# Performance work log

Measured on AMD Instinct MI355X. Metric: run time of the kernel, lower is better.

## Reference

```python
import jax, jax.numpy as jnp
import numpy as np

# ---- static config (from init_kwargs) ----
B_, L_, DM = 4, 2048, 1024
EXPAND, HEADDIM, DSTATE, DCONV = 2, 64, 64, 7
DIN = EXPAND * DM            # 2048
NH = DIN // HEADDIM          # 32
CONV_DIM = DIN + 2 * DSTATE  # 2176 (x, B, C go through the depthwise conv)
DPROJ = 2 * DIN + 2 * DSTATE + 2 * NH  # 4288 (z, xBC, dt_fwd, dt_bwd)
EPS = 1e-5


def setup_inputs() -> dict:
    key = jax.random.key(0)
    ks = jax.random.split(key, 8)
    s = lambda d: 1.0 / np.sqrt(d)
    # dt_bias = inv_softplus(dt) with dt ~ logUniform(1e-3, 0.1)  (Mamba2/Hydra init)
    dt = jnp.exp(jax.random.uniform(ks[3], (NH,)) * (np.log(0.1) - np.log(0.001)) + np.log(0.001))
    return {
        "x": jax.random.normal(ks[0], (B_, L_, DM), jnp.float32),
        "ln_gamma": jnp.ones((DM,), jnp.float32),
        "ln_beta": jnp.zeros((DM,), jnp.float32),
        "W_in": jax.random.normal(ks[1], (DPROJ, DM), jnp.float32) * s(DM),
        "conv_w": jax.random.normal(ks[2], (CONV_DIM, DCONV), jnp.float32) * s(DCONV),
        "conv_b": jnp.zeros((CONV_DIM,), jnp.float32),
        "dt_bias": jnp.log(jnp.expm1(dt)),
        "A_log": jnp.log(jax.random.uniform(ks[4], (NH,), minval=1.0, maxval=16.0)),
        "fc_D_w": jax.random.normal(ks[5], (NH, DIN), jnp.float32) * s(DIN),
        "D": jnp.ones((NH,), jnp.float32),
        "norm_w": jnp.ones((DIN,), jnp.float32),
        "W_out": jax.random.normal(ks[6], (DM, DIN), jnp.float32) * s(DIN),
    }


def _hydra_layer(x, ln_gamma, ln_beta, W_in, conv_w, conv_b, dt_bias, A_log,
                 fc_D_w, D, norm_w, W_out):
    res = x
    # LayerNorm
    mu = jnp.mean(x, -1, keepdims=True)
    var = jnp.mean((x - mu) ** 2, -1, keepdims=True)
    u = (x - mu) * jax.lax.rsqrt(var + EPS) * ln_gamma + ln_beta

    # input projection -> z (gate), xBC (conv stream), dt (fwd+bwd)
    zxbcdt = jnp.einsum('bld,pd->blp', u, W_in)
    z = zxbcdt[..., :DIN]
    xBC = zxbcdt[..., DIN:DIN + CONV_DIM]
    dt = zxbcdt[..., DIN + CONV_DIM:]               # (B,L,2*NH)

    # depthwise 'same' conv along L + SiLU (bidirectional model -> symmetric pad)
    xBC_c = jax.lax.conv_general_dilated(
        xBC.transpose(0, 2, 1), conv_w[:, None, :], (1,),
        [(DCONV // 2, DCONV // 2)], feature_group_count=CONV_DIM)
    xBC = jax.nn.silu((xBC_c + conv_b[None, :, None]).transpose(0, 2, 1))

    xs = xBC[..., :DIN]                             # (B,L,DIN)
    Bm = xBC[..., DIN:DIN + DSTATE]                 # (B,L,N)
    Cm = xBC[..., DIN + DSTATE:]                    # (B,L,N)

    flip = lambda a: a[:, ::-1]
    # stack forward and (flipped) backward direction along batch
    dt2 = jax.nn.softplus(jnp.concatenate([dt[..., :NH], flip(dt[..., NH:])], 0) + dt_bias)  # (2B,L,NH)
    x2 = jnp.concatenate([xs, flip(xs)], 0).reshape(2 * B_, L_, NH, HEADDIM)
    B2 = jnp.concatenate([Bm, flip(Bm)], 0)
    C2 = jnp.concatenate([Cm, flip(Cm)], 0)

    A = -jnp.exp(A_log)                             # (NH,)
    dA = jnp.exp(dt2 * A)                           # (2B,L,NH)

    # selective SSM recurrence: h_t = dA_t * h_{t-1} + dt_t * x_t B_t^T ; y_t = h_t C_t
    def step(h, inp):
        dA_t, dt_t, B_t, C_t, x_t = inp
        dBx = (dt_t[:, :, None, None] * x_t[..., None]) * B_t[:, None, None, :]
        h = dA_t[:, :, None, None] * h + dBx        # (2B,NH,P,N)
        y = jnp.einsum('bhpn,bn->bhp', h, C_t)
        return h, y

    h0 = jnp.zeros((2 * B_, NH, HEADDIM, DSTATE), x.dtype)
    tr = lambda a: jnp.moveaxis(a, 1, 0)
    _, ys = jax.lax.scan(step, h0, (tr(dA), tr(dt2), tr(B2), tr(C2), tr(x2)))
    y = jnp.moveaxis(ys, 0, 1)                      # (2B,L,NH,P)

    # shift by one: strictly off-diagonal part of the quasiseparable mixing matrix
    y = jnp.concatenate([jnp.zeros_like(y[:, :1]), y[:, :-1]], axis=1)
    y = y[:B_] + flip(y[B_:])                       # (B,L,NH,P)

    # data-dependent diagonal: D(x) = fc_D(x) + D, applied per head
    Ddata = jnp.einsum('bld,hd->blh', xs, fc_D_w) + D
    y = y + xs.reshape(B_, L_, NH, HEADDIM) * Ddata[..., None]
    y = y.reshape(B_, L_, DIN)

    # gated RMSNorm (norm after gate)
    y = y * jax.nn.silu(z)
    y = y * jax.lax.rsqrt(jnp.mean(y * y, -1, keepdims=True) + EPS) * norm_w

    # out proj + residual (dropout is identity in eval)
    return res + jnp.einsum('bli,di->bld', y, W_out)


def reference(x, ln_gamma, ln_beta, W_in, conv_w, conv_b, dt_bias, A_log,
              fc_D_w, D, norm_w, W_out):
    return _hydra_layer(x, ln_gamma, ln_beta, W_in, conv_w, conv_b, dt_bias,
                        A_log, fc_D_w, D, norm_w, W_out)
```

## Files before the change

kernel.cpp:

```cpp
#include <hip/hip_runtime.h>
#include <stdint.h>

#define B_   4
#define L_   2048
#define DM   1024
#define DIN  2048
#define NH   32
#define HD   64
#define DSTATE 64
#define DCONV  7
#define CONV_DIM 2176
#define DPROJ 4288
#define NPAD 4352
#define BL   8192
#define EPS  1e-5f
#define QC   128
#define NCH  16

typedef unsigned short u16;
typedef unsigned int   u32;
typedef __bf16 bf16x8 __attribute__((ext_vector_type(8)));
typedef float  f32x4  __attribute__((ext_vector_type(4)));

__device__ __forceinline__ float b2f(u32 b) { return __uint_as_float(b << 16); }
__device__ __forceinline__ u16 f2b(float f) {
    u32 u = __float_as_uint(f);
    u32 r = (u + 0x7fffu + ((u >> 16) & 1u)) >> 16;
    return (u16)r;
}
__device__ __forceinline__ void unpack8(uint4 v, float* f) {
    f[0] = b2f(v.x & 0xffffu); f[1] = b2f(v.x >> 16);
    f[2] = b2f(v.y & 0xffffu); f[3] = b2f(v.y >> 16);
    f[4] = b2f(v.z & 0xffffu); f[5] = b2f(v.z >> 16);
    f[6] = b2f(v.w & 0xffffu); f[7] = b2f(v.w >> 16);
}
__device__ __forceinline__ uint4 pack8(const float* f) {
    uint4 v;
    v.x = (u32)f2b(f[0]) | ((u32)f2b(f[1]) << 16);
    v.y = (u32)f2b(f[2]) | ((u32)f2b(f[3]) << 16);
    v.z = (u32)f2b(f[4]) | ((u32)f2b(f[5]) << 16);
    v.w = (u32)f2b(f[6]) | ((u32)f2b(f[7]) << 16);
    return v;
}
__device__ __forceinline__ int xts(int p, int s) { return p * 136 + ((p >> 3) << 3) + s; }
__device__ __forceinline__ void gload_lds16(const u16* g, u16* l) {
    __builtin_amdgcn_global_load_lds((const __attribute__((address_space(1))) void*)g,
                                     (__attribute__((address_space(3))) void*)l, 16, 0, 0);
}

__global__ __launch_bounds__(256) void k_cvt_win(const float* __restrict__ W, u16* __restrict__ Wb) {
    int idx = blockIdx.x * 256 + threadIdx.x;
    int n = idx >> 10;
    float v = (n < DPROJ) ? W[(size_t)n * DM + (idx & 1023)] : 0.f;
    Wb[idx] = f2b(v);
}
__global__ __launch_bounds__(256) void k_cvt_wout(const float* __restrict__ W, u16* __restrict__ Wb) {
    int idx = blockIdx.x * 256 + threadIdx.x;
    Wb[idx] = f2b(W[idx]);
}
__global__ __launch_bounds__(256) void k_cvt_fcd(const float* __restrict__ W, u16* __restrict__ Wb) {
    int idx = blockIdx.x * 256 + threadIdx.x;
    Wb[idx] = f2b(W[idx]);
}

__global__ __launch_bounds__(256) void k_ln(const float* __restrict__ x, const float* __restrict__ g,
                                            const float* __restrict__ be, u16* __restrict__ u) {
    int row = blockIdx.x, tid = threadIdx.x;
    const float4* xr = (const float4*)(x + (size_t)row * DM);
    float4 v = xr[tid];
    float s1 = v.x + v.y + v.z + v.w;
    float s2 = v.x * v.x + v.y * v.y + v.z * v.z + v.w * v.w;
    for (int o = 32; o; o >>= 1) { s1 += __shfl_down(s1, o); s2 += __shfl_down(s2, o); }
    __shared__ float ls1[4], ls2[4];
    int w = tid >> 6;
    if ((tid & 63) == 0) { ls1[w] = s1; ls2[w] = s2; }
    __syncthreads();
    float t1 = ls1[0] + ls1[1] + ls1[2] + ls1[3];
    float t2 = ls2[0] + ls2[1] + ls2[2] + ls2[3];
    float mu = t1 * (1.f / DM);
    float var = t2 * (1.f / DM) - mu * mu;
    float rs = rsqrtf(var + EPS);
    float4 gv = ((const float4*)g)[tid];
    float4 bv = ((const float4*)be)[tid];
    float o0 = (v.x - mu) * rs * gv.x + bv.x;
    float o1 = (v.y - mu) * rs * gv.y + bv.y;
    float o2 = (v.z - mu) * rs * gv.z + bv.z;
    float o3 = (v.w - mu) * rs * gv.w + bv.w;
    uint2 p;
    p.x = (u32)f2b(o0) | ((u32)f2b(o1) << 16);
    p.y = (u32)f2b(o2) | ((u32)f2b(o3) << 16);
    ((uint2*)(u + (size_t)row * DM))[tid] = p;
}

#define G256_ITER(VMLIT, STG, tcur)                                              \
  {                                                                              \
    asm volatile("s_waitcnt vmcnt(" #VMLIT ")" ::: "memory");                    \
    __builtin_amdgcn_s_barrier();                                                \
    asm volatile("" ::: "memory");                                               \
    const int b_ = (tcur) & 3;                                                   \
    bf16x8 bf_[4], af_[4];                                                       \
    _Pragma("unroll")                                                            \
    for (int nj = 0; nj < 4; nj++) bf_[nj] = *(const bf16x8*)&Bs[b_][rdB + nj * 512]; \
    _Pragma("unroll")                                                            \
    for (int mi = 0; mi < 4; mi++) af_[mi] = *(const bf16x8*)&As[b_][rdA + mi * 512]; \
    if (STG) {                                                                   \
      const int t3_ = (tcur) + 3, b3_ = t3_ & 3, kt3_ = t3_ << 5;                \
      gload_lds16(Ag + arow0 + kt3_, &As[b3_][wiA0 * 512]);                      \
      gload_lds16(Ag + arow1 + kt3_, &As[b3_][wiA1 * 512]);                      \
    }                                                                            \
    __builtin_amdgcn_s_setprio(1);                                               \
    _Pragma("unroll")                                                            \
    for (int mi = 0; mi < 4; mi++)                                               \
      _Pragma("unroll")                                                          \
      for (int nj = 0; nj < 4; nj++)                                             \
        acc[mi][nj] = __builtin_amdgcn_mfma_f32_16x16x32_bf16(af_[mi], bf_[nj], acc[mi][nj], 0, 0, 0); \
    __builtin_amdgcn_s_setprio(0);                                               \
    asm volatile("" ::: "memory");                                               \
    __builtin_amdgcn_s_barrier();                                                \
    asm volatile("" ::: "memory");                                               \
    _Pragma("unroll")                                                            \
    for (int mi = 0; mi < 4; mi++) af_[mi] = *(const bf16x8*)&As[b_][rdA + (4 + mi) * 512]; \
    if (STG) {                                                                   \
      const int t3_ = (tcur) + 3, b3_ = t3_ & 3, kt3_ = t3_ << 5;                \
      gload_lds16(Bg + brow0 + kt3_, &Bs[b3_][wiA0 * 512]);                      \
      gload_lds16(Bg + brow1 + kt3_, &Bs[b3_][wiA1 * 512]);                      \
    }                                                                            \
    __builtin_amdgcn_s_setprio(1);                                               \
    _Pragma("unroll")                                                            \
    for (int mi = 0; mi < 4; mi++)                                               \
      _Pragma("unroll")                                                          \
      for (int nj = 0; nj < 4; nj++)                                             \
        acc[4 + mi][nj] = __builtin_amdgcn_mfma_f32_16x16x32_bf16(af_[mi], bf_[nj], acc[4 + mi][nj], 0, 0, 0); \
    __builtin_amdgcn_s_setprio(0);                                               \
    asm volatile("" ::: "memory");                                               \
    __builtin_amdgcn_sched_barrier(0);                                           \
  }

__global__ __launch_bounds__(512, 2) void k_gemm256(const u16* __restrict__ Ag, const u16* __restrict__ Bg,
                                                    int K, u16* __restrict__ obf, int ldo) {
    __shared__ __align__(16) u16 As[4][8192];
    __shared__ __align__(16) u16 Bs[4][8192];
    const int tid = threadIdx.x;
    const int w = tid >> 6, lane = tid & 63, lr = lane & 15, lq = lane >> 4;
    const int wm = w >> 2, wn = w & 3;
    const int m0 = blockIdx.y * 256, n0 = blockIdx.x * 256;
    const int lrow = lane >> 2;
    const int cs = (lane & 3) ^ ((lane >> 3) & 3);
    const int sAB = (lr >> 1) & 3;
    const int wiA0 = w, wiA1 = w + 8;
    const size_t arow0 = (size_t)(m0 + wiA0 * 16 + lrow) * K + cs * 8;
    const size_t arow1 = (size_t)(m0 + wiA1 * 16 + lrow) * K + cs * 8;
    const size_t brow0 = (size_t)(n0 + wiA0 * 16 + lrow) * K + cs * 8;
    const size_t brow1 = (size_t)(n0 + wiA1 * 16 + lrow) * K + cs * 8;
    const int rdA = (wm * 128 + lr) * 32 + ((lq ^ sAB) << 3);
    const int rdB = (wn * 64 + lr) * 32 + ((lq ^ sAB) << 3);

    f32x4 acc[8][4];
    #pragma unroll
    for (int i = 0; i < 8; i++)
        #pragma unroll
        for (int j = 0; j < 4; j++) acc[i][j] = (f32x4){0.f, 0.f, 0.f, 0.f};

    #pragma unroll
    for (int u = 0; u < 3; u++) {
        gload_lds16(Ag + arow0 + u * 32, &As[u][wiA0 * 512]);
        gload_lds16(Ag + arow1 + u * 32, &As[u][wiA1 * 512]);
        gload_lds16(Bg + brow0 + u * 32, &Bs[u][wiA0 * 512]);
        gload_lds16(Bg + brow1 + u * 32, &Bs[u][wiA1 * 512]);
    }
    const int NT = K >> 5;
    for (int t = 0; t < NT - 3; ++t) G256_ITER(8, 1, t);
    G256_ITER(8, 0, NT - 3);
    G256_ITER(4, 0, NT - 2);
    G256_ITER(0, 0, NT - 1);

    #pragma unroll
    for (int mi = 0; mi < 8; mi++)
        #pragma unroll
        for (int nj = 0; nj < 4; nj++)
            #pragma unroll
            for (int rr = 0; rr < 4; rr++) {
                int m = m0 + wm * 128 + mi * 16 + lq * 4 + rr;
                int n = n0 + wn * 64 + nj * 16 + lr;
                obf[(size_t)m * ldo + n] = f2b(acc[mi][nj][rr]);
            }
}

__global__ __launch_bounds__(256) void k_gemm_bt(const u16* __restrict__ A, const u16* __restrict__ Bw,
                                                 int M, int N, int K, int out_bf16,
                                                 u16* __restrict__ obf, int ldo,
                                                 float* __restrict__ ofp, const float* __restrict__ res) {
    __shared__ __align__(16) u16 As[128 * 64];
    __shared__ __align__(16) u16 Bs[128 * 64];
    int tid = threadIdx.x;
    int m0 = blockIdx.y * 128, n0 = blockIdx.x * 128;
    int w = tid >> 6, lane = tid & 63;
    int wm = (w >> 1) * 64, wn = (w & 1) * 64;
    int lr = lane & 15, lq = lane >> 4;

    f32x4 acc[4][4];
    #pragma unroll
    for (int i = 0; i < 4; i++)
        #pragma unroll
        for (int j = 0; j < 4; j++) acc[i][j] = (f32x4){0.f, 0.f, 0.f, 0.f};

    for (int kt = 0; kt < K; kt += 64) {
        #pragma unroll
        for (int it = 0; it < 4; it++) {
            int s_idx = it * 256 + tid;
            int row = s_idx >> 3;
            int kcg = (s_idx & 7) ^ (row & 7);
            u16* lbase_a = &As[(it * 256 + w * 64) * 8];
            u16* lbase_b = &Bs[(it * 256 + w * 64) * 8];
            gload_lds16(A + (size_t)(m0 + row) * K + kt + kcg * 8, lbase_a);
            gload_lds16(Bw + (size_t)(n0 + row) * K + kt + kcg * 8, lbase_b);
        }
        __syncthreads();
        #pragma unroll
        for (int kk = 0; kk < 2; kk++) {
            bf16x8 af[4], bfr[4];
            #pragma unroll
            for (int i = 0; i < 4; i++) {
                int row = wm + 16 * i + lr;
                af[i] = *(const bf16x8*)&As[row * 64 + (((kk * 4 + lq)) ^ (row & 7)) * 8];
            }
            #pragma unroll
            for (int j = 0; j < 4; j++) {
                int row = wn + 16 * j + lr;
                bfr[j] = *(const bf16x8*)&Bs[row * 64 + (((kk * 4 + lq)) ^ (row & 7)) * 8];
            }
            #pragma unroll
            for (int i = 0; i < 4; i++)
                #pragma unroll
                for (int j = 0; j < 4; j++)
                    acc[i][j] = __builtin_amdgcn_mfma_f32_16x16x32_bf16(af[i], bfr[j], acc[i][j], 0, 0, 0);
        }
        __syncthreads();
    }
    #pragma unroll
    for (int i = 0; i < 4; i++) {
        #pragma unroll
        for (int j = 0; j < 4; j++) {
            #pragma unroll
            for (int rr = 0; rr < 4; rr++) {
                int m = m0 + wm + 16 * i + lq * 4 + rr;
                int n = n0 + wn + 16 * j + lr;
                float v = acc[i][j][rr];
                if (out_bf16) obf[(size_t)m * ldo + n] = f2b(v);
                else          ofp[(size_t)m * ldo + n] = v + res[(size_t)m * ldo + n];
            }
        }
    }
}

__global__ __launch_bounds__(256) void k_dproj(const u16* __restrict__ xs, const u16* __restrict__ fcb,
                                               const float* __restrict__ Dv, float* __restrict__ Dd) {
    __shared__ __align__(16) u16 As[32 * 72];
    __shared__ __align__(16) u16 Bs[32 * 72];
    int tid = threadIdx.x;
    int m0 = blockIdx.x * 32;
    int w = tid >> 6, lane = tid & 63, lr = lane & 15, lq = lane >> 4;
    int mt = (w & 1) * 16, nt = (w >> 1) * 16;
    int r = tid >> 3, kc = tid & 7;
    f32x4 acc = (f32x4){0.f, 0.f, 0.f, 0.f};
    for (int kt = 0; kt < DIN; kt += 64) {
        *(uint4*)&As[r * 72 + kc * 8] = *(const uint4*)(xs + (size_t)(m0 + r) * DIN + kt + kc * 8);
        *(uint4*)&Bs[r * 72 + kc * 8] = *(const uint4*)(fcb + (size_t)r * DIN + kt + kc * 8);
        __syncthreads();
        #pragma unroll
        for (int ks = 0; ks < 2; ks++) {
            bf16x8 a = *(const bf16x8*)&As[(mt + lr) * 72 + ks * 32 + lq * 8];
            bf16x8 b = *(const bf16x8*)&Bs[(nt + lr) * 72 + ks * 32 + lq * 8];
            acc = __builtin_amdgcn_mfma_f32_16x16x32_bf16(a, b, acc, 0, 0, 0);
        }
        __syncthreads();
    }
    #pragma unroll
    for (int rr = 0; rr < 4; rr++) {
        int m = m0 + mt + lq * 4 + rr;
        int n = nt + lr;
        Dd[(size_t)m * 32 + n] = acc[rr] + Dv[n];
    }
}

__global__ __launch_bounds__(256) void k_conv(const u16* __restrict__ zx, const float* __restrict__ cw,
                                              const float* __restrict__ cb, u16* __restrict__ xs,
                                              u16* __restrict__ BCb) {
    __shared__ u16 sh[262 * 64];
    int c0 = blockIdx.x * 64, t0 = blockIdx.y * 256, b = blockIdx.z;
    int tid = threadIdx.x;
    int c = tid & 63, tg = tid >> 6;
    for (int it = 0; it < 66; it++) {
        int r = it * 4 + tg;
        if (r < 262) {
            int t = t0 + r - 3;
            u16 v = 0;
            if (t >= 0 && t < L_) v = zx[(size_t)(b * L_ + t) * NPAD + DIN + c0 + c];
            sh[r * 64 + c] = v;
        }
    }
    float wgt[7];
    #pragma unroll
    for (int k = 0; k < 7; k++) wgt[k] = cw[(c0 + c) * 7 + k];
    float bias = cb[c0 + c];
    __syncthreads();
    int cg = c0 + c;
    for (int tt = 0; tt < 64; tt++) {
        int tl = tt * 4 + tg;
        float a = bias;
        #pragma unroll
        for (int k = 0; k < 7; k++) a += b2f(sh[(tl + k) * 64 + c]) * wgt[k];
        float v = a / (1.f + __expf(-a));
        size_t row = (size_t)b * L_ + (t0 + tl);
        if (cg < DIN) xs[row * DIN + cg] = f2b(v);
        else          BCb[row * 128 + (cg - DIN)] = f2b(v);
    }
}

__global__ __launch_bounds__(256) void k_chunk(const u16* __restrict__ xs, const u16* __restrict__ BCb,
                                               const u16* __restrict__ zx, const float* __restrict__ dt_bias,
                                               const float* __restrict__ A_log, u16* __restrict__ y0,
                                               u16* __restrict__ y1, float* __restrict__ wout,
                                               float* __restrict__ decay, u16* __restrict__ scb) {
    __shared__ __align__(16) u16 ab[18432];
    __shared__ __align__(16) u16 XT[8768];
    __shared__ __align__(16) u16 BT[8768];
    __shared__ __align__(16) float dts_s[128];
    __shared__ __align__(16) float lda_s[128];
    __shared__ __align__(16) float wend[128];
    __shared__ __align__(16) double cumd[128];

    const int blk = blockIdx.x;
    const int c = blk & 15, dbh = blk >> 4;
    const int h = dbh & 31, b = (dbh >> 5) & 3, dir = dbh >> 7;
    const int tid = threadIdx.x, w = tid >> 6, lane = tid & 63, lr = lane & 15, lq = lane >> 4;
    const int s0 = c * QC;
    u16* yo = dir ? y1 : y0;

    if (tid < 128) {
        int s = s0 + tid;
        int t = dir ? (L_ - 1 - s) : s;
        float draw = b2f(zx[(size_t)(b * L_ + t) * NPAD + (DIN + CONV_DIM) + dir * 32 + h]);
        float xb = draw + dt_bias[h];
        float dt2 = (xb > 20.f) ? xb : log1pf(__expf(xb));
        dts_s[tid] = dt2;
        lda_s[tid] = -__expf(A_log[h]) * dt2;
    }
    {
        int sl0 = tid >> 3, ng = (tid & 7) * 8;
        #pragma unroll
        for (int it = 0; it < 4; it++) {
            int sl = sl0 + it * 32;
            int s = s0 + sl;
            int t = dir ? (L_ - 1 - s) : s;
            size_t row = (size_t)b * L_ + t;
            const u16* bcr = BCb + row * 128;
            uint4 cv = *(const uint4*)(bcr + 64 + ng);
            *(uint4*)&ab[sl * 72 + ng] = cv;
            uint4 pb = *(const uint4*)(bcr + ng);
            *(uint4*)&ab[9216 + sl * 72 + ng] = pb;
            u16 bh[8] = {(u16)(pb.x & 0xffffu), (u16)(pb.x >> 16), (u16)(pb.y & 0xffffu), (u16)(pb.y >> 16),
                         (u16)(pb.z & 0xffffu), (u16)(pb.z >> 16), (u16)(pb.w & 0xffffu), (u16)(pb.w >> 16)};
            #pragma unroll
            for (int i = 0; i < 8; i++) BT[(ng + i) * 136 + ng + sl] = bh[i];
            uint4 xv = *(const uint4*)(xs + row * DIN + h * 64 + ng);
            u16 xh[8] = {(u16)(xv.x & 0xffffu), (u16)(xv.x >> 16), (u16)(xv.y & 0xffffu), (u16)(xv.y >> 16),
                         (u16)(xv.z & 0xffffu), (u16)(xv.z >> 16), (u16)(xv.w & 0xffffu), (u16)(xv.w >> 16)};
            #pragma unroll
            for (int i = 0; i < 8; i++) XT[(ng + i) * 136 + ng + sl] = xh[i];
        }
    }
    __syncthreads();
    if (w == 0) {
        double v0 = (double)lda_s[lane];
        double v1 = (double)lda_s[64 + lane];
        #pragma unroll
        for (int o = 1; o < 64; o <<= 1) {
            double t0 = __shfl_up(v0, o);
            double t1 = __shfl_up(v1, o);
            if (lane >= o) { v0 += t0; v1 += t1; }
        }
        double tot0 = __shfl(v0, 63);
        cumd[lane] = v0;
        cumd[64 + lane] = tot0 + v1;
    }
    bf16x8 af[2][2];
    #pragma unroll
    for (int ti = 0; ti < 2; ti++)
        #pragma unroll
        for (int ks = 0; ks < 2; ks++)
            af[ti][ks] = *(const bf16x8*)&ab[(w * 32 + ti * 16 + lr) * 72 + ks * 32 + lq * 8];
    f32x4 accg[2][8];
    #pragma unroll
    for (int ti = 0; ti < 2; ti++)
        #pragma unroll
        for (int si = 0; si < 8; si++) accg[ti][si] = (f32x4){0.f, 0.f, 0.f, 0.f};
    #pragma unroll
    for (int si = 0; si < 8; si++)
        #pragma unroll
        for (int ks = 0; ks < 2; ks++) {
            bf16x8 bf = *(const bf16x8*)&ab[9216 + (si * 16 + lr) * 72 + ks * 32 + lq * 8];
            accg[0][si] = __builtin_amdgcn_mfma_f32_16x16x32_bf16(af[0][ks], bf, accg[0][si], 0, 0, 0);
            accg[1][si] = __builtin_amdgcn_mfma_f32_16x16x32_bf16(af[1][ks], bf, accg[1][si], 0, 0, 0);
        }
    __syncthreads();
    if (tid < 128) wend[tid] = __expf((float)(cumd[127] - cumd[tid])) * dts_s[tid];
    {
        double cumt_d[8];
        #pragma unroll
        for (int ti = 0; ti < 2; ti++)
            #pragma unroll
            for (int r = 0; r < 4; r++) cumt_d[ti * 4 + r] = cumd[w * 32 + ti * 16 + lq * 4 + r];
        double cums_d[8]; float dts_l[8];
        #pragma unroll
        for (int si = 0; si < 8; si++) { cums_d[si] = cumd[si * 16 + lr]; dts_l[si] = dts_s[si * 16 + lr]; }
        #pragma unroll
        for (int ti = 0; ti < 2; ti++)
            #pragma unroll
            for (int si = 0; si < 8; si++)
                #pragma unroll
                for (int r = 0; r < 4; r++) {
                    int t_l = w * 32 + ti * 16 + lq * 4 + r;
                    int s_l = si * 16 + lr;
                    float v = 0.f;
                    if (s_l <= t_l)
                        v = __expf((float)(cumt_d[ti * 4 + r] - cums_d[si])) * dts_l[si] * accg[ti][si][r];
                    ab[xts(t_l, s_l)] = f2b(v);
                }
    }
    __syncthreads();
    f32x4 acc[2][4];
    #pragma unroll
    for (int ti = 0; ti < 2; ti++)
        #pragma unroll
        for (int pj = 0; pj < 4; pj++) acc[ti][pj] = (f32x4){0.f, 0.f, 0.f, 0.f};
    #pragma unroll
    for (int ks = 0; ks < 4; ks++) {
        bf16x8 a0 = *(const bf16x8*)&ab[xts(w * 32 + lr, ks * 32 + lq * 8)];
        bf16x8 a1 = *(const bf16x8*)&ab[xts(w * 32 + 16 + lr, ks * 32 + lq * 8)];
        #pragma unroll
        for (int pj = 0; pj < 4; pj++) {
            bf16x8 bf = *(const bf16x8*)&XT[xts(pj * 16 + lr, ks * 32 + lq * 8)];
            acc[0][pj] = __builtin_amdgcn_mfma_f32_16x16x32_bf16(a0, bf, acc[0][pj], 0, 0, 0);
            acc[1][pj] = __builtin_amdgcn_mfma_f32_16x16x32_bf16(a1, bf, acc[1][pj], 0, 0, 0);
        }
    }
    #pragma unroll
    for (int ti = 0; ti < 2; ti++)
        #pragma unroll
        for (int pj = 0; pj < 4; pj++)
            #pragma unroll
            for (int r = 0; r < 4; r++) {
                int t_l = w * 32 + ti * 16 + lq * 4 + r;
                int s = s0 + t_l;
                int t = dir ? (L_ - 1 - s) : s;
                yo[((size_t)b * L_ + t) * DIN + h * 64 + pj * 16 + lr] = f2b(acc[ti][pj][r]);
            }
    f32x4 accs[4];
    #pragma unroll
    for (int nj = 0; nj < 4; nj++) accs[nj] = (f32x4){0.f, 0.f, 0.f, 0.f};
    #pragma unroll
    for (int ks = 0; ks < 4; ks++) {
        uint4 xv = *(const uint4*)&XT[xts(w * 16 + lr, ks * 32 + lq * 8)];
        float xf[8]; unpack8(xv, xf);
        float4 w0 = *(const float4*)&wend[ks * 32 + lq * 8];
        float4 w1 = *(const float4*)&wend[ks * 32 + lq * 8 + 4];
        float fs[8] = {xf[0]*w0.x, xf[1]*w0.y, xf[2]*w0.z, xf[3]*w0.w,
                       xf[4]*w1.x, xf[5]*w1.y, xf[6]*w1.z, xf[7]*w1.w};
        bf16x8 a = __builtin_bit_cast(bf16x8, pack8(fs));
        #pragma unroll
        for (int nj = 0; nj < 4; nj++) {
            bf16x8 bb = *(const bf16x8*)&BT[xts(nj * 16 + lr, ks * 32 + lq * 8)];
            accs[nj] = __builtin_amdgcn_mfma_f32_16x16x32_bf16(a, bb, accs[nj], 0, 0, 0);
        }
    }
    #pragma unroll
    for (int nj = 0; nj < 4; nj++)
        #pragma unroll
        for (int r = 0; r < 4; r++) {
            int p = w * 16 + lq * 4 + r, n = nj * 16 + lr;
            scb[(size_t)blk * 4096 + p * 64 + n] = f2b(accs[nj][r]);
        }
    if (tid < 128) wout[dbh * 2048 + s0 + tid] = __expf((float)cumd[tid]);
    if (tid == 0)  decay[blk] = __expf((float)cumd[127]);
}

__global__ __launch_bounds__(256) void k_hscan(const float* __restrict__ decay, u16* __restrict__ scb) {
    int dbh = blockIdx.x, tid = threadIdx.x;
    u16* base = scb + (size_t)dbh * 16 * 4096 + tid * 16;
    float hcur[16];
    #pragma unroll
    for (int i = 0; i < 16; i++) hcur[i] = 0.f;
    for (int c = 0; c < NCH; c++) {
        u16* sg = base + (size_t)c * 4096;
        uint4 q0 = *(const uint4*)sg;
        uint4 q1 = *(const uint4*)(sg + 8);
        float sf[16]; unpack8(q0, sf); unpack8(q1, sf + 8);
        *(uint4*)sg       = pack8(hcur);
        *(uint4*)(sg + 8) = pack8(hcur + 8);
        float dk = decay[dbh * 16 + c];
        #pragma unroll
        for (int i = 0; i < 16; i++) hcur[i] = dk * hcur[i] + sf[i];
    }
}

__global__ __launch_bounds__(256) void k_inter(const u16* __restrict__ BCb, const float* __restrict__ wout,
                                               const u16* __restrict__ hin, u16* __restrict__ y0,
                                               u16* __restrict__ y1) {
    __shared__ __align__(16) u16 Csc[128 * 72];
    __shared__ __align__(16) u16 hs[64 * 72];
    const int blk = blockIdx.x;
    const int c = blk & 15, dbh = blk >> 4;
    const int h = dbh & 31, b = (dbh >> 5) & 3, dir = dbh >> 7;
    const int tid = threadIdx.x, w = tid >> 6, lane = tid & 63, lr = lane & 15, lq = lane >> 4;
    u16* yo = dir ? y1 : y0;

    {
        int g = tid * 16, p = g >> 6, n = g & 63;
        const u16* hg = hin + (size_t)blk * 4096 + g;
        *(uint4*)&hs[p * 72 + n]     = *(const uint4*)hg;
        *(uint4*)&hs[p * 72 + n + 8] = *(const uint4*)(hg + 8);
    }
    const int sl0 = tid >> 3, ng = (tid & 7) * 8;
    #pragma unroll
    for (int it = 0; it < 4; it++) {
        int sl = sl0 + it * 32;
        int s = c * QC + sl;
        int t = dir ? (L_ - 1 - s) : s;
        const u16* bcr = BCb + ((size_t)b * L_ + t) * 128 + 64 + ng;
        float sc = wout[dbh * 2048 + s];
        uint4 cv = *(const uint4*)bcr;
        float cf[8]; unpack8(cv, cf);
        float f[8] = {cf[0]*sc, cf[1]*sc, cf[2]*sc, cf[3]*sc, cf[4]*sc, cf[5]*sc, cf[6]*sc, cf[7]*sc};
        *(uint4*)&Csc[sl * 72 + ng] = pack8(f);
    }
    __syncthreads();
    f32x4 acc[2][4];
    #pragma unroll
    for (int ti = 0; ti < 2; ti++)
        #pragma unroll
        for (int pj = 0; pj < 4; pj++) acc[ti][pj] = (f32x4){0.f, 0.f, 0.f, 0.f};
    #pragma unroll
    for (int ks = 0; ks < 2; ks++) {
        bf16x8 a0 = *(const bf16x8*)&Csc[(w * 32 + lr) * 72 + ks * 32 + lq * 8];
        bf16x8 a1 = *(const bf16x8*)&Csc[(w * 32 + 16 + lr) * 72 + ks * 32 + lq * 8];
        #pragma unroll
        for (int pj = 0; pj < 4; pj++) {
            bf16x8 bb = *(const bf16x8*)&hs[(pj * 16 + lr) * 72 + ks * 32 + lq * 8];
            acc[0][pj] = __builtin_amdgcn_mfma_f32_16x16x32_bf16(a0, bb, acc[0][pj], 0, 0, 0);
            acc[1][pj] = __builtin_amdgcn_mfma_f32_16x16x32_bf16(a1, bb, acc[1][pj], 0, 0, 0);
        }
    }
    #pragma unroll
    for (int ti = 0; ti < 2; ti++)
        #pragma unroll
        for (int pj = 0; pj < 4; pj++)
            #pragma unroll
            for (int r = 0; r < 4; r++) {
                int t_l = w * 32 + ti * 16 + lq * 4 + r;
                int s = c * QC + t_l;
                int t = dir ? (L_ - 1 - s) : s;
                u16* yp = yo + ((size_t)b * L_ + t) * DIN + h * 64 + pj * 16 + lr;
                *yp = f2b(acc[ti][pj][r] + b2f(*yp));
            }
}

__global__ __launch_bounds__(256) void k_gate(const u16* __restrict__ xs, const u16* __restrict__ zx,
                                              const u16* __restrict__ y0, const u16* __restrict__ y1,
                                              const float* __restrict__ Dd,
                                              const float* __restrict__ nw, u16* __restrict__ yn) {
    int row = blockIdx.x, tid = threadIdx.x;
    int t = row & (L_ - 1);
    __shared__ float red[4];
    size_t base = (size_t)row * DIN;
    uint4 xv = ((const uint4*)(xs + base))[tid];
    uint4 zv = ((const uint4*)(zx + (size_t)row * NPAD))[tid];
    uint4 zero4 = {0u, 0u, 0u, 0u};
    uint4 a0 = (t > 0)      ? ((const uint4*)(y0 + base - DIN))[tid] : zero4;
    uint4 a1 = (t < L_ - 1) ? ((const uint4*)(y1 + base + DIN))[tid] : zero4;
    float sD = Dd[(size_t)row * 32 + (tid >> 3)];
    float xf[8], zf[8], f0[8], f1[8];
    unpack8(xv, xf); unpack8(zv, zf); unpack8(a0, f0); unpack8(a1, f1);
    int d0 = tid * 8;
    float g[8]; float ss = 0.f;
    #pragma unroll
    for (int i = 0; i < 8; i++) {
        float yv = f0[i] + f1[i] + xf[i] * sD;
        float z = zf[i];
        float gg = yv * (z / (1.f + __expf(-z)));
        g[i] = gg; ss += gg * gg;
    }
    for (int o = 32; o; o >>= 1) ss += __shfl_down(ss, o);
    if ((tid & 63) == 0) red[tid >> 6] = ss;
    __syncthreads();
    float tot = red[0] + red[1] + red[2] + red[3];
    float r = rsqrtf(tot * (1.f / DIN) + EPS);
    float o8[8];
    #pragma unroll
    for (int i = 0; i < 8; i++) o8[i] = g[i] * r * nw[d0 + i];
    ((uint4*)(yn + base))[tid] = pack8(o8);
}

#define OFF_U     ((size_t)0)
#define OFF_WIN   ((size_t)16777216)
#define OFF_WOUT  ((size_t)25690112)
#define OFF_ZX    ((size_t)29884416)
#define OFF_XS    ((size_t)101187584)
#define OFF_BC    ((size_t)134742016)
#define OFF_DTA   ((size_t)138936320)
#define OFF_Y0    ((size_t)143130624)
#define OFF_Y1    ((size_t)176685056)
#define OFF_YN    ((size_t)210239488)
#define OFF_WO2   OFF_U
#define OFF_DEC   (OFF_U + 2097152)
#define OFF_FCB   (OFF_U + 2113536)
#define OFF_DD    (OFF_U + 2244608)
#define OFF_SCB   OFF_YN

extern "C" void kernel_launch(void* const* d_in, const int* in_sizes, int n_in,
                              void* d_out, int out_size, void* d_ws, size_t ws_size,
                              hipStream_t stream) {
    const float* x       = (const float*)d_in[0];
    const float* ln_g    = (const float*)d_in[1];
    const float* ln_b    = (const float*)d_in[2];
    const float* W_in    = (const float*)d_in[3];
    const float* conv_w  = (const float*)d_in[4];
    const float* conv_b  = (const float*)d_in[5];
    const float* dt_bias = (const float*)d_in[6];
    const float* A_log   = (const float*)d_in[7];
    const float* fc_D_w  = (const float*)d_in[8];
    const float* Dv      = (const float*)d_in[9];
    const float* norm_w  = (const float*)d_in[10];
    const float* W_out   = (const float*)d_in[11];

    char* ws = (char*)d_ws;
    u16*   u_bf  = (u16*)(ws + OFF_U);
    u16*   winb  = (u16*)(ws + OFF_WIN);
    u16*   woutb = (u16*)(ws + OFF_WOUT);
    u16*   zx    = (u16*)(ws + OFF_ZX);
    u16*   xs    = (u16*)(ws + OFF_XS);
    u16*   BCb   = (u16*)(ws + OFF_BC);
    u16*   y0b   = (u16*)(ws + OFF_Y0);
    u16*   y1b   = (u16*)(ws + OFF_Y1);
    u16*   ynb   = (u16*)(ws + OFF_YN);
    float* wo2   = (float*)(ws + OFF_WO2);
    float* dec   = (float*)(ws + OFF_DEC);
    u16*   fcb   = (u16*)(ws + OFF_FCB);
    float* Dd    = (float*)(ws + OFF_DD);
    u16*   scb   = (u16*)(ws + OFF_SCB);

    k_cvt_win <<<(NPAD * DM) / 256, 256, 0, stream>>>(W_in, winb);
    k_cvt_wout<<<(DM * DIN) / 256, 256, 0, stream>>>(W_out, woutb);
    k_ln      <<<BL, 256, 0, stream>>>(x, ln_g, ln_b, u_bf);
    k_gemm256 <<<dim3(NPAD / 256, BL / 256), 512, 0, stream>>>(u_bf, winb, DM, zx, NPAD);
    k_cvt_fcd <<<(NH * DIN) / 256, 256, 0, stream>>>(fc_D_w, fcb);
    k_conv    <<<dim3(CONV_DIM / 64, L_ / 256, B_), 256, 0, stream>>>(zx, conv_w, conv_b, xs, BCb);
    k_dproj   <<<BL / 32, 256, 0, stream>>>(xs, fcb, Dv, Dd);
    k_chunk   <<<4096, 256, 0, stream>>>(xs, BCb, zx, dt_bias, A_log, y0b, y1b, wo2, dec, scb);
    k_hscan   <<<256, 256, 0, stream>>>(dec, scb);
    k_inter   <<<4096, 256, 0, stream>>>(BCb, wo2, scb, y0b, y1b);
    k_gate    <<<BL, 256, 0, stream>>>(xs, zx, y0b, y1b, Dd, norm_w, ynb);
    k_gemm_bt <<<dim3(DM / 128, BL / 128), 256, 0, stream>>>(ynb, woutb, BL, DM, DIN, 0, nullptr, DM, (float*)d_out, x);
}
```

Measured before the change: 537.5 us.

## Double-buffer LDS fragment registers in 256 GEMM to overlap reads with MFMA

Restructures the k_gemm256 main loop so that the LDS fragment reads for the next k-tile are issued into a second register set (even/odd) before the MFMAs of the current tile, with one barrier per tile instead of two. Global-to-LDS staging of A and B for tile t+3 is issued together at the start of each step. This aims to hide LDS read latency behind the matrix instructions and halve the barrier count, at the cost of roughly twice as many live fragment registers, which could cause spills or lower occupancy under the 512x2 launch bounds.

```diff
diff --git a/kernel.cpp b/kernel.cpp
--- a/kernel.cpp
+++ b/kernel.cpp
@@ -92,49 +92,35 @@
     ((uint2*)(u + (size_t)row * DM))[tid] = p;
 }
 
-#define G256_ITER(VMLIT, STG, tcur)                                              \
-  {                                                                              \
-    asm volatile("s_waitcnt vmcnt(" #VMLIT ")" ::: "memory");                    \
+#define G2_STAGE(tnext)                                                          \
+  { const int b3_ = (tnext) & 3, kt3_ = (tnext) << 5;                            \
+    gload_lds16(Ag + arow0 + kt3_, &As[b3_][wiA0 * 512]);                        \
+    gload_lds16(Ag + arow1 + kt3_, &As[b3_][wiA1 * 512]);                        \
+    gload_lds16(Bg + brow0 + kt3_, &Bs[b3_][wiA0 * 512]);                        \
+    gload_lds16(Bg + brow1 + kt3_, &Bs[b3_][wiA1 * 512]); }
+
+#define G2_WAITBAR(VM)                                                           \
+  { asm volatile("s_waitcnt vmcnt(" #VM ")" ::: "memory");                       \
     __builtin_amdgcn_s_barrier();                                                \
-    asm volatile("" ::: "memory");                                               \
-    const int b_ = (tcur) & 3;                                                   \
-    bf16x8 bf_[4], af_[4];                                                       \
+    asm volatile("" ::: "memory"); }
+
+#define G2_READ(tr, AF, BF)                                                      \
+  { const int b_ = (tr) & 3;                                                     \
     _Pragma("unroll")                                                            \
-    for (int nj = 0; nj < 4; nj++) bf_[nj] = *(const bf16x8*)&Bs[b_][rdB + nj * 512]; \
+    for (int nj = 0; nj < 4; nj++) BF[nj] = *(const bf16x8*)&Bs[b_][rdB + nj * 512]; \
     _Pragma("unroll")                                                            \
-    for (int mi = 0; mi < 4; mi++) af_[mi] = *(const bf16x8*)&As[b_][rdA + mi * 512]; \
-    if (STG) {                                                                   \
-      const int t3_ = (tcur) + 3, b3_ = t3_ & 3, kt3_ = t3_ << 5;                \
-      gload_lds16(Ag + arow0 + kt3_, &As[b3_][wiA0 * 512]);                      \
-      gload_lds16(Ag + arow1 + kt3_, &As[b3_][wiA1 * 512]);                      \
-    }                                                                            \
+    for (int mi = 0; mi < 8; mi++) AF[mi] = *(const bf16x8*)&As[b_][rdA + mi * 512]; }
+
+#define G2_MFMA(AF, BF)                                                          \
+  { __builtin_amdgcn_sched_barrier(0);                                           \
     __builtin_amdgcn_s_setprio(1);                                               \
     _Pragma("unroll")                                                            \
-    for (int mi = 0; mi < 4; mi++)                                               \
+    for (int mi = 0; mi < 8; mi++)                                               \
       _Pragma("unroll")                                                          \
       for (int nj = 0; nj < 4; nj++)                                             \
-        acc[mi][nj] = __builtin_amdgcn_mfma_f32_16x16x32_bf16(af_[mi], bf_[nj], acc[mi][nj], 0, 0, 0); \
+        acc[mi][nj] = __builtin_amdgcn_mfma_f32_16x16x32_bf16(AF[mi], BF[nj], acc[mi][nj], 0, 0, 0); \
     __builtin_amdgcn_s_setprio(0);                                               \
-    asm volatile("" ::: "memory");                                               \
-    __builtin_amdgcn_s_barrier();                                                \
-    asm volatile("" ::: "memory");                                               \
-    _Pragma("unroll")                                                            \
-    for (int mi = 0; mi < 4; mi++) af_[mi] = *(const bf16x8*)&As[b_][rdA + (4 + mi) * 512]; \
-    if (STG) {                                                                   \
-      const int t3_ = (tcur) + 3, b3_ = t3_ & 3, kt3_ = t3_ << 5;                \
-      gload_lds16(Bg + brow0 + kt3_, &Bs[b3_][wiA0 * 512]);                      \
-      gload_lds16(Bg + brow1 + kt3_, &Bs[b3_][wiA1 * 512]);                      \
-    }                                                                            \
-    __builtin_amdgcn_s_setprio(1);                                               \
-    _Pragma("unroll")                                                            \
-    for (int mi = 0; mi < 4; mi++)                                               \
-      _Pragma("unroll")                                                          \
-      for (int nj = 0; nj < 4; nj++)                                             \
-        acc[4 + mi][nj] = __builtin_amdgcn_mfma_f32_16x16x32_bf16(af_[mi], bf_[nj], acc[4 + mi][nj], 0, 0, 0); \
-    __builtin_amdgcn_s_setprio(0);                                               \
-    asm volatile("" ::: "memory");                                               \
-    __builtin_amdgcn_sched_barrier(0);                                           \
-  }
+    asm volatile("" ::: "memory"); }
 
 __global__ __launch_bounds__(512, 2) void k_gemm256(const u16* __restrict__ Ag, const u16* __restrict__ Bg,
                                                     int K, u16* __restrict__ obf, int ldo) {
@@ -161,18 +147,34 @@
         #pragma unroll
         for (int j = 0; j < 4; j++) acc[i][j] = (f32x4){0.f, 0.f, 0.f, 0.f};
 
-    #pragma unroll
-    for (int u = 0; u < 3; u++) {
-        gload_lds16(Ag + arow0 + u * 32, &As[u][wiA0 * 512]);
-        gload_lds16(Ag + arow1 + u * 32, &As[u][wiA1 * 512]);
-        gload_lds16(Bg + brow0 + u * 32, &Bs[u][wiA0 * 512]);
-        gload_lds16(Bg + brow1 + u * 32, &Bs[u][wiA1 * 512]);
-    }
+    bf16x8 afE[8], bfE[4], afO[8], bfO[4];
+
+    G2_STAGE(0); G2_STAGE(1); G2_STAGE(2);
+    G2_WAITBAR(8);
+    G2_READ(0, afE, bfE);
+
     const int NT = K >> 5;
-    for (int t = 0; t < NT - 3; ++t) G256_ITER(8, 1, t);
-    G256_ITER(8, 0, NT - 3);
-    G256_ITER(4, 0, NT - 2);
-    G256_ITER(0, 0, NT - 1);
+    for (int t = 0; t < NT - 4; t += 2) {
+        G2_STAGE(t + 3);
+        G2_WAITBAR(8);
+        G2_READ(t + 1, afO, bfO);
+        G2_MFMA(afE, bfE);
+        G2_STAGE(t + 4);
+        G2_WAITBAR(8);
+        G2_READ(t + 2, afE, bfE);
+        G2_MFMA(afO, bfO);
+    }
+    G2_STAGE(NT - 1);
+    G2_WAITBAR(8);
+    G2_READ(NT - 3, afO, bfO);
+    G2_MFMA(afE, bfE);
+    G2_WAITBAR(4);
+    G2_READ(NT - 2, afE, bfE);
+    G2_MFMA(afO, bfO);
+    G2_WAITBAR(0);
+    G2_READ(NT - 1, afO, bfO);
+    G2_MFMA(afE, bfE);
+    G2_MFMA(afO, bfO);
 
     #pragma unroll
     for (int mi = 0; mi < 8; mi++)
```

After: 534.5 us. No clear change (-0.6%).
